# Performance work log

Hardware: AMD Instinct MI355X
Metric: run time of the kernel (lower is better)

Reference implementation:

```python
import jax, jax.numpy as jnp
import numpy as np

NUCLEIC_ACID_CUTOFF = 30.0
OTHER_CUTOFF = 15.0


def _cdist(x):
    # x: [b, n, 3] -> pairwise euclidean distances [b, n, n]
    sq = jnp.sum(x * x, axis=-1)  # [b, n]
    d2 = sq[:, :, None] + sq[:, None, :] - 2.0 * jnp.einsum('bid,bjd->bij', x, x)
    d2 = jnp.maximum(d2, 0.0)
    # safe sqrt (zero diagonal would produce nan grads otherwise)
    safe = jnp.where(d2 > 0.0, d2, 1.0)
    return jnp.where(d2 > 0.0, jnp.sqrt(safe), 0.0)


def setup_inputs() -> dict:
    key = jax.random.key(0)
    k1, k2, k3, k4, k5 = jax.random.split(key, 5)
    b, n = 2, 4096
    # scale ~10 Angstrom spread so distances straddle the 15/30 cutoffs
    true_coords = jax.random.normal(k1, (b, n, 3), dtype=jnp.float32) * 10.0
    pred_coords = true_coords + jax.random.normal(k2, (b, n, 3), dtype=jnp.float32) * 1.5
    is_dna = jax.random.bernoulli(k3, 0.15, (b, n))
    is_rna = jax.random.bernoulli(k4, 0.15, (b, n))
    coords_mask = jax.random.bernoulli(k5, 0.95, (b, n))
    return {
        'pred_coords': pred_coords,
        'true_coords': true_coords,
        'is_dna': is_dna,
        'is_rna': is_rna,
        'coords_mask': coords_mask,
    }


def reference(pred_coords, true_coords, is_dna, is_rna, coords_mask):
    n = pred_coords.shape[1]
    pred_dists = _cdist(pred_coords)  # [b, n, n]
    true_dists = _cdist(true_coords)  # [b, n, n]
    dist_diff = jnp.abs(true_dists - pred_dists)
    eps = (
        jax.nn.sigmoid(0.5 - dist_diff)
        + jax.nn.sigmoid(1.0 - dist_diff)
        + jax.nn.sigmoid(2.0 - dist_diff)
        + jax.nn.sigmoid(4.0 - dist_diff)
    ) / 4.0

    is_nucleotide = is_dna | is_rna  # [b, n]
    is_nucleotide_pair = is_nucleotide[:, :, None] & is_nucleotide[:, None, :]
    inclusion_radius = jnp.where(
        is_nucleotide_pair,
        true_dists < NUCLEIC_ACID_CUTOFF,
        true_dists < OTHER_CUTOFF,
    )
    not_eye = ~jnp.eye(n, dtype=bool)[None, :, :]
    mask = inclusion_radius & not_eye
    mask = mask & (coords_mask[:, :, None] & coords_mask[:, None, :])

    maskf = mask.astype(eps.dtype)
    lddt_sum = jnp.sum(eps * maskf, axis=(-1, -2))  # [b]
    lddt_count = jnp.sum(maskf, axis=(-1, -2))  # [b]
    lddt = lddt_sum / jnp.maximum(lddt_count, 1.0)
    return 1.0 - jnp.mean(lddt)
```

## Files before the change

### kernel.cpp

```cpp
#include <hip/hip_runtime.h>
#include <hip/hip_bf16.h>


#define NRES 4096
#define NBATCH 2
#define TJ 64
#define NACT 544
#define NBLOCKS (NACT * NBATCH)

#define CUT15 21.6404256133f
#define CUT30 43.2808512267f

#define S1 66.35420923f
#define S2 678.60880385f
#define S3 2039.58217570f
#define S4 1808.04241445f
#define QP1 16.58855231f
#define QP2 339.30440193f
#define QP3 1529.68663177f
#define QP4 1808.04241445f

#define LOG2E 1.44269504089f

__global__ void pack_kernel(const float* __restrict__ pred,
                            const float* __restrict__ truec,
                            const int* __restrict__ dna,
                            const int* __restrict__ rna,
                            const int* __restrict__ cm,
                            float4* __restrict__ tp,
                            float4* __restrict__ pp)
{
    int idx = blockIdx.x * 256 + threadIdx.x;
    if (idx >= NRES * NBATCH) return;
    float nuc = ((dna[idx] | rna[idx]) != 0) ? 1.0f : 0.0f;
    float cmf = (cm[idx] != 0) ? 1.0f : 0.0f;
    tp[idx] = make_float4(truec[3*idx+0]*LOG2E, truec[3*idx+1]*LOG2E, truec[3*idx+2]*LOG2E, nuc);
    pp[idx] = make_float4(pred[3*idx+0]*LOG2E,  pred[3*idx+1]*LOG2E,  pred[3*idx+2]*LOG2E,  cmf);
}

#define K_LOOP(DIAG)                                                        \
    _Pragma("unroll 4")                                                     \
    for (int k = 0; k < TJ; ++k) {                                          \
        const float4 tj = stj[k];                                           \
        const float4 pj = spj[k];                                           \
        float dx = tix - tj.x, dy = tiy - tj.y, dz = tiz - tj.z;            \
        float dt = __builtin_amdgcn_sqrtf(dx*dx + dy*dy + dz*dz);           \
        float ex = pix - pj.x, ey = piy - pj.y, ez = piz - pj.z;            \
        float dp = __builtin_amdgcn_sqrtf(ex*ex + ey*ey + ez*ez);           \
        float cutoff = __builtin_fmaf(tj.w, cHiLo, cLo);                    \
        float mf = (dt < cutoff) ? pj.w : 0.0f;                             \
        if (DIAG) mf = (j0 + k > i) ? mf : 0.0f;                            \
        float t = __builtin_amdgcn_exp2f(-fabsf(dt - dp));                  \
        float Q  = 1.0f + t*(S1 + t*(S2 + t*(S3 + t*S4)));                  \
        float Qp = QP1 + t*(QP2 + t*(QP3 + t*QP4));                         \
        float rq = __builtin_amdgcn_rcpf(Q);                                \
        s += mf * ((t * Qp) * rq);                                          \
        c += mf;                                                            \
    }

__launch_bounds__(256, 6)
__global__ void lddt_main(const float4* __restrict__ tp,
                          const float4* __restrict__ pp,
                          float* __restrict__ acc,
                          unsigned int* __restrict__ done,
                          float* __restrict__ out)
{
    const int b   = blockIdx.y;
    const int m   = blockIdx.x;
    const int tid = threadIdx.x;

    int bi = 0, C = 0;
    while (C + (TJ - 4 * bi) <= m) { C += TJ - 4 * bi; ++bi; }
    const int cj = 4 * bi + (m - C);

    const int base = b * NRES;
    const int j0   = cj * TJ;
    const int i    = bi * 256 + tid;

    __shared__ float4 stj[TJ];
    __shared__ float4 spj[TJ];
    if (tid < TJ)                stj[tid]      = tp[base + j0 + tid];
    else if (tid < 2 * TJ)       spj[tid - TJ] = pp[base + j0 + (tid - TJ)];

    const float4 ti4 = tp[base + i];
    const float4 pi4 = pp[base + i];
    const float tix = ti4.x, tiy = ti4.y, tiz = ti4.z;
    const float pix = pi4.x, piy = pi4.y, piz = pi4.z;
    const bool  cmi  = (pi4.w != 0.0f);
    const bool  nuci = (ti4.w != 0.0f);
    const float cHi = cmi ? (nuci ? CUT30 : CUT15) : -1.0f;
    const float cLo = cmi ? CUT15 : -1.0f;
    const float cHiLo = cHi - cLo;

    __syncthreads();

    float s = 0.0f, c = 0.0f;

    if (cj < 4 * bi + 4) { K_LOOP(1) }
    else                 { K_LOOP(0) }

    #pragma unroll
    for (int off = 32; off > 0; off >>= 1) {
        s += __shfl_down(s, off, 64);
        c += __shfl_down(c, off, 64);
    }

    __shared__ float red_s[4];
    __shared__ float red_c[4];
    const int wid  = tid >> 6;
    const int lane = tid & 63;
    if (lane == 0) { red_s[wid] = s; red_c[wid] = c; }
    __syncthreads();

    if (tid == 0) {
        float ts = red_s[0] + red_s[1] + red_s[2] + red_s[3];
        float tc = red_c[0] + red_c[1] + red_c[2] + red_c[3];
        atomicAdd(&acc[b], ts);
        atomicAdd(&acc[NBATCH + b], tc);
        __threadfence();
        unsigned int old = atomicAdd(done, 1u);
        if (old == NBLOCKS - 1u) {
            float a0 = __hip_atomic_load(&acc[0], __ATOMIC_ACQUIRE, __HIP_MEMORY_SCOPE_AGENT);
            float a1 = __hip_atomic_load(&acc[1], __ATOMIC_ACQUIRE, __HIP_MEMORY_SCOPE_AGENT);
            float c0 = __hip_atomic_load(&acc[2], __ATOMIC_ACQUIRE, __HIP_MEMORY_SCOPE_AGENT);
            float c1 = __hip_atomic_load(&acc[3], __ATOMIC_ACQUIRE, __HIP_MEMORY_SCOPE_AGENT);
            float l0 = a0 / fmaxf(c0, 0.5f);
            float l1 = a1 / fmaxf(c1, 0.5f);
            out[0] = 1.0f - 0.5f * (l0 + l1);
        }
    }
}

extern "C" void kernel_launch(void* const* d_in, const int* in_sizes, int n_in,
                              void* d_out, int out_size, void* d_ws, size_t ws_size,
                              hipStream_t stream) {
    const float* pred  = (const float*)d_in[0];
    const float* truec = (const float*)d_in[1];
    const int*   dna   = (const int*)d_in[2];
    const int*   rna   = (const int*)d_in[3];
    const int*   cmask = (const int*)d_in[4];
    float* out = (float*)d_out;

    char* ws = (char*)d_ws;
    float*        acc  = (float*)ws;
    unsigned int* done = (unsigned int*)(ws + 64);
    float4* tp = (float4*)(ws + 1024);
    float4* pp = (float4*)(ws + 1024 + NBATCH*NRES*16);

    (void)hipMemsetAsync(ws, 0, 128, stream);

    pack_kernel<<<(NRES*NBATCH + 255)/256, 256, 0, stream>>>(pred, truec, dna, rna, cmask, tp, pp);

    dim3 grid(NACT, NBATCH);
    lddt_main<<<grid, 256, 0, stream>>>(tp, pp, acc, done, out);
}
```

Before: 52.03 us.

## Convert pair kernel to persistent blocks pulling 1024x32 tiles from an atomic queue

The one-block-per-tile grid of 256x64 tiles is replaced by 256 persistent 1024-thread blocks. Each block claims triangular 1024x32 tiles from a global atomic counter and accumulates per-batch partial sums in registers. Each block then reduces once and issues one set of atomics, so far fewer blocks launch and hit the global accumulators. In exchange, 640 tiles over 256 blocks leaves a partial last round that can idle CUs, and each tile needs an atomic fetch plus two block barriers.

```diff
diff --git a/kernel.cpp b/kernel.cpp
--- a/kernel.cpp
+++ b/kernel.cpp
@@ -4,9 +4,11 @@
 
 #define NRES 4096
 #define NBATCH 2
-#define TJ 64
-#define NACT 544
-#define NBLOCKS (NACT * NBATCH)
+#define TIB 1024
+#define TJ 32
+#define NTILE_B 320
+#define NTILES (NTILE_B * NBATCH)
+#define NPBLK 256
 
 #define CUT15 21.6404256133f
 #define CUT30 43.2808512267f
@@ -55,77 +57,100 @@
         float Qp = QP1 + t*(QP2 + t*(QP3 + t*QP4));                         \
         float rq = __builtin_amdgcn_rcpf(Q);                                \
         s += mf * ((t * Qp) * rq);                                          \
-        c += mf;                                                            \
+        cc += mf;                                                           \
     }
 
-__launch_bounds__(256, 6)
+__launch_bounds__(1024, 4)
 __global__ void lddt_main(const float4* __restrict__ tp,
                           const float4* __restrict__ pp,
                           float* __restrict__ acc,
+                          unsigned int* __restrict__ work,
                           unsigned int* __restrict__ done,
                           float* __restrict__ out)
 {
-    const int b   = blockIdx.y;
-    const int m   = blockIdx.x;
-    const int tid = threadIdx.x;
-
-    int bi = 0, C = 0;
-    while (C + (TJ - 4 * bi) <= m) { C += TJ - 4 * bi; ++bi; }
-    const int cj = 4 * bi + (m - C);
-
-    const int base = b * NRES;
-    const int j0   = cj * TJ;
-    const int i    = bi * 256 + tid;
+    const int tid  = threadIdx.x;
+    const int wid  = tid >> 6;
+    const int lane = tid & 63;
 
     __shared__ float4 stj[TJ];
     __shared__ float4 spj[TJ];
-    if (tid < TJ)                stj[tid]      = tp[base + j0 + tid];
-    else if (tid < 2 * TJ)       spj[tid - TJ] = pp[base + j0 + (tid - TJ)];
+    __shared__ unsigned int sm;
 
-    const float4 ti4 = tp[base + i];
-    const float4 pi4 = pp[base + i];
-    const float tix = ti4.x, tiy = ti4.y, tiz = ti4.z;
-    const float pix = pi4.x, piy = pi4.y, piz = pi4.z;
-    const bool  cmi  = (pi4.w != 0.0f);
-    const bool  nuci = (ti4.w != 0.0f);
-    const float cHi = cmi ? (nuci ? CUT30 : CUT15) : -1.0f;
-    const float cLo = cmi ? CUT15 : -1.0f;
-    const float cHiLo = cHi - cLo;
+    float s0 = 0.0f, c0 = 0.0f, s1 = 0.0f, c1 = 0.0f;
 
-    __syncthreads();
+    for (;;) {
+        if (tid == 0) sm = atomicAdd(work, 1u);
+        __syncthreads();
+        const unsigned int m = sm;
+        if (m >= NTILES) break;
 
-    float s = 0.0f, c = 0.0f;
+        const int b  = (m >= NTILE_B) ? 1 : 0;
+        const int mm = m - b * NTILE_B;
+        int bi, cj;
+        if      (mm < 128) { bi = 0; cj = mm; }
+        else if (mm < 224) { bi = 1; cj = 32 + (mm - 128); }
+        else if (mm < 288) { bi = 2; cj = 64 + (mm - 224); }
+        else               { bi = 3; cj = 96 + (mm - 288); }
 
-    if (cj < 4 * bi + 4) { K_LOOP(1) }
-    else                 { K_LOOP(0) }
+        const int base = b * NRES;
+        const int j0   = cj * TJ;
+
+        if (tid < TJ)          stj[tid]      = tp[base + j0 + tid];
+        else if (tid < 2 * TJ) spj[tid - TJ] = pp[base + j0 + (tid - TJ)];
+
+        const int i = bi * TIB + tid;
+        const float4 ti4 = tp[base + i];
+        const float4 pi4 = pp[base + i];
+        const float tix = ti4.x, tiy = ti4.y, tiz = ti4.z;
+        const float pix = pi4.x, piy = pi4.y, piz = pi4.z;
+        const bool  cmi  = (pi4.w != 0.0f);
+        const bool  nuci = (ti4.w != 0.0f);
+        const float cHi = cmi ? (nuci ? CUT30 : CUT15) : -1.0f;
+        const float cLo = cmi ? CUT15 : -1.0f;
+        const float cHiLo = cHi - cLo;
+
+        __syncthreads();
+
+        float s = 0.0f, cc = 0.0f;
+        if (cj < 32 * bi + 32) { K_LOOP(1) }
+        else                   { K_LOOP(0) }
+
+        if (b) { s1 += s; c1 += cc; }
+        else   { s0 += s; c0 += cc; }
+    }
 
     #pragma unroll
     for (int off = 32; off > 0; off >>= 1) {
-        s += __shfl_down(s, off, 64);
-        c += __shfl_down(c, off, 64);
+        s0 += __shfl_down(s0, off, 64);
+        c0 += __shfl_down(c0, off, 64);
+        s1 += __shfl_down(s1, off, 64);
+        c1 += __shfl_down(c1, off, 64);
     }
 
-    __shared__ float red_s[4];
-    __shared__ float red_c[4];
-    const int wid  = tid >> 6;
-    const int lane = tid & 63;
-    if (lane == 0) { red_s[wid] = s; red_c[wid] = c; }
+    __shared__ float red[16][4];
+    if (lane == 0) { red[wid][0] = s0; red[wid][1] = c0; red[wid][2] = s1; red[wid][3] = c1; }
     __syncthreads();
 
     if (tid == 0) {
-        float ts = red_s[0] + red_s[1] + red_s[2] + red_s[3];
-        float tc = red_c[0] + red_c[1] + red_c[2] + red_c[3];
-        atomicAdd(&acc[b], ts);
-        atomicAdd(&acc[NBATCH + b], tc);
+        float ts0 = 0, tc0 = 0, ts1 = 0, tc1 = 0;
+        #pragma unroll
+        for (int w = 0; w < 16; ++w) {
+            ts0 += red[w][0]; tc0 += red[w][1];
+            ts1 += red[w][2]; tc1 += red[w][3];
+        }
+        atomicAdd(&acc[0], ts0);
+        atomicAdd(&acc[2], tc0);
+        atomicAdd(&acc[1], ts1);
+        atomicAdd(&acc[3], tc1);
         __threadfence();
         unsigned int old = atomicAdd(done, 1u);
-        if (old == NBLOCKS - 1u) {
+        if (old == NPBLK - 1u) {
             float a0 = __hip_atomic_load(&acc[0], __ATOMIC_ACQUIRE, __HIP_MEMORY_SCOPE_AGENT);
             float a1 = __hip_atomic_load(&acc[1], __ATOMIC_ACQUIRE, __HIP_MEMORY_SCOPE_AGENT);
-            float c0 = __hip_atomic_load(&acc[2], __ATOMIC_ACQUIRE, __HIP_MEMORY_SCOPE_AGENT);
-            float c1 = __hip_atomic_load(&acc[3], __ATOMIC_ACQUIRE, __HIP_MEMORY_SCOPE_AGENT);
-            float l0 = a0 / fmaxf(c0, 0.5f);
-            float l1 = a1 / fmaxf(c1, 0.5f);
+            float cc0 = __hip_atomic_load(&acc[2], __ATOMIC_ACQUIRE, __HIP_MEMORY_SCOPE_AGENT);
+            float cc1 = __hip_atomic_load(&acc[3], __ATOMIC_ACQUIRE, __HIP_MEMORY_SCOPE_AGENT);
+            float l0 = a0 / fmaxf(cc0, 0.5f);
+            float l1 = a1 / fmaxf(cc1, 0.5f);
             out[0] = 1.0f - 0.5f * (l0 + l1);
         }
     }
@@ -144,6 +169,7 @@
     char* ws = (char*)d_ws;
     float*        acc  = (float*)ws;
     unsigned int* done = (unsigned int*)(ws + 64);
+    unsigned int* work = (unsigned int*)(ws + 96);
     float4* tp = (float4*)(ws + 1024);
     float4* pp = (float4*)(ws + 1024 + NBATCH*NRES*16);
 
@@ -151,6 +177,5 @@
 
     pack_kernel<<<(NRES*NBATCH + 255)/256, 256, 0, stream>>>(pred, truec, dna, rna, cmask, tp, pp);
 
-    dim3 grid(NACT, NBATCH);
-    lddt_main<<<grid, 256, 0, stream>>>(tp, pp, acc, done, out);
+    lddt_main<<<NPBLK, 1024, 0, stream>>>(tp, pp, acc, work, done, out);
 }
```

New measurement: 48.07 us. 7.6% less time.
